# Optimization experiments

Hardware: AMD Instinct MI355X
Metric: run time of the kernel (lower is better)

## Reference

```python
import jax, jax.numpy as jnp
import numpy as np

BS, S, D, H, DFF, L = 8, 1024, 256, 8, 1024, 3
DK = D // H
NEG = -1e32


def setup_inputs() -> dict:
    key = jax.random.key(0)
    ks = jax.random.split(key, 10)
    r = lambda k, shp: jax.random.normal(k, shp, jnp.float32) * 0.02
    return {
        "q_embed_data": jax.random.normal(ks[0], (BS, S, D), jnp.float32),
        "qa_embed_data": jax.random.normal(ks[1], (BS, S, D), jnp.float32),
        "Wk": r(ks[2], (L, D, D)), "bk": jnp.zeros((L, D), jnp.float32),
        "Wv": r(ks[3], (L, D, D)), "bv": jnp.zeros((L, D), jnp.float32),
        "Wo": r(ks[4], (L, D, D)), "bo": jnp.zeros((L, D), jnp.float32),
        "gammas": r(ks[5], (L, H)),
        "ln1_g": jnp.ones((L, D), jnp.float32), "ln1_b": jnp.zeros((L, D), jnp.float32),
        "W1": r(ks[6], (L, D, DFF)), "b1": jnp.zeros((L, DFF), jnp.float32),
        "W2": r(ks[7], (L, DFF, D)), "b2": jnp.zeros((L, D), jnp.float32),
        "ln2_g": jnp.ones((L, D), jnp.float32), "ln2_b": jnp.zeros((L, D), jnp.float32),
    }


def _layernorm(x, g, b, eps=1e-5):
    mu = x.mean(-1, keepdims=True)
    var = ((x - mu) ** 2).mean(-1, keepdims=True)
    return (x - mu) * jax.lax.rsqrt(var + eps) * g + b


def _attn(xq, xk, xv, Wk, bk, Wv, bv, Wo, bo, gamma, mask, zero_pad):
    # kq_same=1: q and k both use k_linear
    bs = xq.shape[0]
    q = (xq @ Wk + bk).reshape(bs, S, H, DK).transpose(0, 2, 1, 3)  # bhsd
    k = (xk @ Wk + bk).reshape(bs, S, H, DK).transpose(0, 2, 1, 3)
    v = (xv @ Wv + bv).reshape(bs, S, H, DK).transpose(0, 2, 1, 3)
    scores = jnp.einsum('bhid,bhjd->bhij', q, k) / np.float32(np.sqrt(DK))
    mf = mask.astype(scores.dtype)
    # no-grad decay branch (detached in torch)
    p = jax.nn.softmax(jnp.where(mask, scores, NEG), axis=-1) * mf
    distcum = jnp.cumsum(p, axis=-1)
    disttot = p.sum(axis=-1, keepdims=True)
    idx = jnp.arange(S)
    pos = jnp.abs(idx[None, :] - idx[:, None]).astype(jnp.float32)[None, None]
    dist = jnp.sqrt(jnp.clip((disttot - distcum) * pos, 0.0, None))
    dist = jax.lax.stop_gradient(dist)
    g = -jax.nn.softplus(gamma)[None, :, None, None]  # (1,H,1,1)
    total_effect = jnp.clip(jnp.exp(dist * g), 1e-5, 1e5)
    scores = scores * total_effect
    attn = jax.nn.softmax(jnp.where(mask, scores, NEG), axis=-1)
    if zero_pad:
        attn = attn.at[:, :, 0, :].set(0.0)
    out = jnp.einsum('bhij,bhjd->bhid', attn, v)
    out = out.transpose(0, 2, 1, 3).reshape(bs, S, D)
    return out @ Wo + bo


def _block(i, xq, xk, xv, mask, zero_pad, apply_pos, P):
    Wk, bk, Wv, bv, Wo, bo, gam, l1g, l1b, W1, b1, W2, b2, l2g, l2b = [p[i] for p in P]
    q2 = _attn(xq, xk, xv, Wk, bk, Wv, bv, Wo, bo, gam, mask, zero_pad)
    x = _layernorm(xq + q2, l1g, l1b)
    if apply_pos:
        ff = jax.nn.relu(x @ W1 + b1) @ W2 + b2
        x = _layernorm(x + ff, l2g, l2b)
    return x


def _forward(q_embed_data, qa_embed_data, Wk, bk, Wv, bv, Wo, bo, gammas,
             ln1_g, ln1_b, W1, b1, W2, b2, ln2_g, ln2_b):
    P = (Wk, bk, Wv, bv, Wo, bo, gammas, ln1_g, ln1_b, W1, b1, W2, b2, ln2_g, ln2_b)
    tri_incl = jnp.tril(jnp.ones((S, S), bool))[None, None]       # mask=1: peek current+past
    tri_excl = jnp.tril(jnp.ones((S, S), bool), -1)[None, None]   # mask=0: strictly past
    x, y = q_embed_data, qa_embed_data
    # blocks_1 (n_blocks=1): mask=1, apply_pos=True, self-attn on y
    y = _block(0, y, y, y, tri_incl, False, True, P)
    # blocks_2 (2*n_blocks=2): alternate (mask=1, no FFN) / (mask=0, zero_pad, FFN, values=y)
    x = _block(1, x, x, x, tri_incl, False, False, P)
    x = _block(2, x, x, y, tri_excl, True, True, P)
    return x


def reference(q_embed_data, qa_embed_data, Wk, bk, Wv, bv, Wo, bo, gammas,
              ln1_g, ln1_b, W1, b1, W2, b2, ln2_g, ln2_b):
    return _forward(q_embed_data, qa_embed_data, Wk, bk, Wv, bv, Wo, bo, gammas,
                    ln1_g, ln1_b, W1, b1, W2, b2, ln2_g, ln2_b)
```

## Files before the change

### kernel.cpp

```cpp
#include <hip/hip_runtime.h>

typedef unsigned short u16;
typedef float f32x4 __attribute__((ext_vector_type(4)));
typedef __bf16 bf16x8 __attribute__((ext_vector_type(8)));
typedef u16 u16x8 __attribute__((ext_vector_type(8)));
typedef u16 u16x4 __attribute__((ext_vector_type(4)));
typedef __fp16 h16x2 __attribute__((ext_vector_type(2)));

__device__ __forceinline__ u16 f2bf(float f) {
  union { float f; unsigned u; } v; v.f = f;
  unsigned r = (v.u + 0x7FFFu + ((v.u >> 16) & 1u)) >> 16;
  return (u16)r;
}
__device__ __forceinline__ unsigned cvtpk_bf16(float lo, float hi) {
  unsigned r;
  asm("v_cvt_pk_bf16_f32 %0, %1, %2" : "=v"(r) : "v"(lo), "v"(hi));
  return r;
}
__device__ __forceinline__ unsigned pk_f16(float a, float b) {
  union { h16x2 h; unsigned u; } v;
  v.h = __builtin_amdgcn_cvt_pkrtz(a, b);
  return v.u;
}
__device__ __forceinline__ float2 unpk_f16(unsigned u) {
  union { unsigned u; h16x2 h; } v; v.u = u;
  return make_float2((float)v.h.x, (float)v.h.y);
}
__device__ __forceinline__ float wred_sum(float v) {
#pragma unroll
  for (int o = 32; o >= 1; o >>= 1) v += __shfl_xor(v, o);
  return v;
}

template <int RELU, int WF32, int WBF, int WVT>
__global__ __launch_bounds__(256) void gemm_kernel(
    const u16* __restrict__ A, const u16* __restrict__ Bt,
    const float* __restrict__ bias, float* __restrict__ C,
    u16* __restrict__ Cbf, int M, int N, int K) {
  __shared__ u16 As[64 * 64];
  __shared__ u16 Bs[64 * 64];
  const int tid = threadIdx.x;
  const int lane = tid & 63;
  const int w = tid >> 6;
  const int m0 = blockIdx.x * 64;
  const int n0 = blockIdx.y * 64;
  const int wr = (w >> 1) * 32;
  const int wc = (w & 1) * 32;
  const int l15 = lane & 15, hi = lane >> 4;

  f32x4 acc[2][2] = {};

  for (int k0 = 0; k0 < K; k0 += 64) {
#pragma unroll
    for (int rep = 0; rep < 2; ++rep) {
      int idx = tid + rep * 256;
      int row = idx >> 3, c8 = idx & 7;
      int cs = ((c8 ^ (row & 7)) << 3);
      __builtin_amdgcn_global_load_lds(
          (const __attribute__((address_space(1))) void*)(A + (size_t)(m0 + row) * K + k0 + cs),
          (__attribute__((address_space(3))) void*)(&As[idx * 8]), 16, 0, 0);
      __builtin_amdgcn_global_load_lds(
          (const __attribute__((address_space(1))) void*)(Bt + (size_t)(n0 + row) * K + k0 + cs),
          (__attribute__((address_space(3))) void*)(&Bs[idx * 8]), 16, 0, 0);
    }
    __syncthreads();
#pragma unroll
    for (int kk = 0; kk < 2; ++kk) {
      int kb = (kk * 32 + (hi << 3)) << 1;
      bf16x8 af[2], bfr[2];
#pragma unroll
      for (int mf = 0; mf < 2; ++mf) {
        int m = wr + mf * 16 + l15;
        af[mf] = *(const bf16x8*)((const char*)As + m * 128 + (kb ^ ((m & 7) << 4)));
      }
#pragma unroll
      for (int nf = 0; nf < 2; ++nf) {
        int n = wc + nf * 16 + l15;
        bfr[nf] = *(const bf16x8*)((const char*)Bs + n * 128 + (kb ^ ((n & 7) << 4)));
      }
#pragma unroll
      for (int mf = 0; mf < 2; ++mf)
#pragma unroll
        for (int nf = 0; nf < 2; ++nf)
          acc[mf][nf] = __builtin_amdgcn_mfma_f32_16x16x32_bf16(af[mf], bfr[nf], acc[mf][nf], 0, 0, 0);
    }
    __syncthreads();
  }

#pragma unroll
  for (int mf = 0; mf < 2; ++mf)
#pragma unroll
    for (int nf = 0; nf < 2; ++nf) {
      int col = n0 + wc + nf * 16 + l15;
      float bia = bias[col];
      u16x4 tv;
#pragma unroll
      for (int r = 0; r < 4; ++r) {
        int row = m0 + wr + mf * 16 + (hi << 2) + r;
        float val = acc[mf][nf][r] + bia;
        if (RELU) val = fmaxf(val, 0.f);
        if (WF32) C[(size_t)row * N + col] = val;
        if (WBF) Cbf[(size_t)row * N + col] = f2bf(val);
        if (WVT) tv[r] = f2bf(val);
      }
      if (WVT) {
        int row0 = m0 + wr + mf * 16 + (hi << 2);
        size_t addr = (((size_t)(row0 >> 10) * 8 + (col >> 5)) * 32 + (col & 31)) * 1024 + (row0 & 1023);
        *(u16x4*)(Cbf + addr) = tv;
      }
    }
}

__global__ __launch_bounds__(256) void gemm_kv_kernel(
    const u16* __restrict__ A, const u16* __restrict__ Bt,
    const float* __restrict__ biasK, const float* __restrict__ biasV,
    u16* __restrict__ qkbf, u16* __restrict__ vT, int M, int N, int K) {
  __shared__ u16 As[64 * 64];
  __shared__ u16 Bs[64 * 64];
  const int tid = threadIdx.x;
  const int lane = tid & 63;
  const int w = tid >> 6;
  const int m0 = blockIdx.x * 64;
  const int n0 = blockIdx.y * 64;
  const int wr = (w >> 1) * 32;
  const int wc = (w & 1) * 32;
  const int l15 = lane & 15, hi = lane >> 4;

  f32x4 acc[2][2] = {};

  for (int k0 = 0; k0 < K; k0 += 64) {
#pragma unroll
    for (int rep = 0; rep < 2; ++rep) {
      int idx = tid + rep * 256;
      int row = idx >> 3, c8 = idx & 7;
      int cs = ((c8 ^ (row & 7)) << 3);
      __builtin_amdgcn_global_load_lds(
          (const __attribute__((address_space(1))) void*)(A + (size_t)(m0 + row) * K + k0 + cs),
          (__attribute__((address_space(3))) void*)(&As[idx * 8]), 16, 0, 0);
      __builtin_amdgcn_global_load_lds(
          (const __attribute__((address_space(1))) void*)(Bt + (size_t)(n0 + row) * K + k0 + cs),
          (__attribute__((address_space(3))) void*)(&Bs[idx * 8]), 16, 0, 0);
    }
    __syncthreads();
#pragma unroll
    for (int kk = 0; kk < 2; ++kk) {
      int kb = (kk * 32 + (hi << 3)) << 1;
      bf16x8 af[2], bfr[2];
#pragma unroll
      for (int mf = 0; mf < 2; ++mf) {
        int m = wr + mf * 16 + l15;
        af[mf] = *(const bf16x8*)((const char*)As + m * 128 + (kb ^ ((m & 7) << 4)));
      }
#pragma unroll
      for (int nf = 0; nf < 2; ++nf) {
        int n = wc + nf * 16 + l15;
        bfr[nf] = *(const bf16x8*)((const char*)Bs + n * 128 + (kb ^ ((n & 7) << 4)));
      }
#pragma unroll
      for (int mf = 0; mf < 2; ++mf)
#pragma unroll
        for (int nf = 0; nf < 2; ++nf)
          acc[mf][nf] = __builtin_amdgcn_mfma_f32_16x16x32_bf16(af[mf], bfr[nf], acc[mf][nf], 0, 0, 0);
    }
    __syncthreads();
  }

  const bool isV = (n0 >= 256);
#pragma unroll
  for (int mf = 0; mf < 2; ++mf)
#pragma unroll
    for (int nf = 0; nf < 2; ++nf) {
      int col = n0 + wc + nf * 16 + l15;
      float bia = isV ? biasV[col - 256] : biasK[col];
      u16x4 tv;
#pragma unroll
      for (int r = 0; r < 4; ++r) {
        int row = m0 + wr + mf * 16 + (hi << 2) + r;
        float val = acc[mf][nf][r] + bia;
        if (!isV) qkbf[(size_t)row * 256 + col] = f2bf(val);
        tv[r] = f2bf(val);
      }
      if (isV) {
        int row0 = m0 + wr + mf * 16 + (hi << 2);
        int vc = col - 256;
        size_t addr = (((size_t)(row0 >> 10) * 8 + (vc >> 5)) * 32 + (vc & 31)) * 1024 + (row0 & 1023);
        *(u16x4*)(vT + addr) = tv;
      }
    }
}

__global__ __launch_bounds__(256) void attn_mfma_kernel(
    const u16* __restrict__ qkbf, const u16* __restrict__ vT,
    u16* __restrict__ ao, const float* __restrict__ gam, int excl) {
  __shared__ float zbuf[4][16];
  __shared__ float z2buf[4][16];
  __shared__ float accbuf[8][4][64];

  const int lane = threadIdx.x & 63, w = threadIdx.x >> 6;
  const int qt = 63 - blockIdx.y;
  const int bh = blockIdx.x;
  const int b = bh >> 3, h = bh & 7;
  const int q0 = qt * 16;
  const int l15 = lane & 15, hi = lane >> 4;
  const int i = q0 + l15;
  const float LOG2E = 1.4426950408889634f;
  const float g2 = -log1pf(__expf(gam[h])) * LOG2E;
  const float cscale = 0.17677669529663687f * LOG2E;
  const float CLIP2 = -16.609640474436812f;

  const u16* kbase = qkbf + ((size_t)b * 1024) * 256 + h * 32;
  const bf16x8 qfrag = *(const bf16x8*)(kbase + (size_t)i * 256 + hi * 8);

  const int mylim = i - excl;
  const int jmax = q0 + 15 - excl;
  const int ntiles = (jmax >> 4) + 1;
  const int C = (ntiles + 3) >> 2;
  const int c0 = w * C;
  const int tEnd = (c0 + C < ntiles) ? (c0 + C) : ntiles;
  const int count = (tEnd > c0) ? (tEnd - c0) : 0;

  unsigned lpk[32];
  float zacc = 0.f;
#pragma unroll
  for (int tl = 0; tl < 16; ++tl) {
    if (tl < count) {
      const int t = c0 + tl;
      bf16x8 kf = *(const bf16x8*)(kbase + (size_t)(t * 16 + l15) * 256 + hi * 8);
      f32x4 sA = {};
      sA = __builtin_amdgcn_mfma_f32_16x16x32_bf16(kf, qfrag, sA, 0, 0, 0);
      float l0 = sA[0] * cscale, l1 = sA[1] * cscale;
      float l2 = sA[2] * cscale, l3 = sA[3] * cscale;
      if (t == ntiles - 1) {
        const int kb = t * 16 + hi * 4;
        l0 = (kb + 0 <= mylim) ? l0 : -1000.f;
        l1 = (kb + 1 <= mylim) ? l1 : -1000.f;
        l2 = (kb + 2 <= mylim) ? l2 : -1000.f;
        l3 = (kb + 3 <= mylim) ? l3 : -1000.f;
      }
      zacc += (exp2f(l0) + exp2f(l1)) + (exp2f(l2) + exp2f(l3));
      lpk[2 * tl] = pk_f16(l0, l1);
      lpk[2 * tl + 1] = pk_f16(l2, l3);
    } else {
      lpk[2 * tl] = 0xE3D0E3D0u;
      lpk[2 * tl + 1] = 0xE3D0E3D0u;
    }
  }
  zacc += __shfl_xor(zacc, 16);
  zacc += __shfl_xor(zacc, 32);
  if (lane < 16) zbuf[w][lane] = zacc;
  __syncthreads();

  const float zc0 = zbuf[0][l15], zc1 = zbuf[1][l15];
  const float zc2 = zbuf[2][l15], zc3 = zbuf[3][l15];
  const float Z = zc0 + zc1 + zc2 + zc3;
  const float invZ = Z > 0.f ? 1.f / Z : 0.f;
  float prefix = 0.f;
  if (w > 0) prefix += zc0;
  if (w > 1) prefix += zc1;
  if (w > 2) prefix += zc2;

  const u16* vbase = vT + (size_t)bh * 32 * 1024;
  float carry = prefix, z2 = 0.f;
  f32x4 accO0 = {}, accO1 = {};
  const int Cp = (count + 1) & ~1;

  auto tile_sm = [&](int tlocal, unsigned pa, unsigned pb,
                     unsigned& u0, unsigned& u1) {
    float2 v01 = unpk_f16(pa), v23 = unpk_f16(pb);
    const float l0 = v01.x, l1 = v01.y, l2 = v23.x, l3 = v23.y;
    const float e0 = exp2f(l0), e1 = exp2f(l1);
    const float e2 = exp2f(l2), e3 = exp2f(l3);
    const float cA = e0 + e1, cB = cA + e2, cC = cB + e3;
    float vsc = cC;
    float tmp = __shfl_up(vsc, 16); if (hi >= 1) vsc += tmp;
    tmp = __shfl_up(vsc, 32); if (hi >= 2) vsc += tmp;
    const float exg = vsc - cC;
    const float tot = __shfl(vsc, l15 + 48);
    const float cb = carry + exg;
    carry += tot;
    const int kb = (c0 + tlocal) * 16 + hi * 4;
    const float posb = (float)(i - kb);
    const float r0 = (Z - (cb + e0)) * invZ;
    const float r1 = (Z - (cb + cA)) * invZ;
    const float r2 = (Z - (cb + cB)) * invZ;
    const float r3 = (Z - (cb + cC)) * invZ;
    const float d20 = fmaxf(r0 * posb, 0.f);
    const float d21 = fmaxf(r1 * (posb - 1.f), 0.f);
    const float d22 = fmaxf(r2 * (posb - 2.f), 0.f);
    const float d23 = fmaxf(r3 * (posb - 3.f), 0.f);
    const float a0 = fmaxf(__builtin_amdgcn_sqrtf(d20) * g2, CLIP2);
    const float a1 = fmaxf(__builtin_amdgcn_sqrtf(d21) * g2, CLIP2);
    const float a2 = fmaxf(__builtin_amdgcn_sqrtf(d22) * g2, CLIP2);
    const float a3 = fmaxf(__builtin_amdgcn_sqrtf(d23) * g2, CLIP2);
    const float p0 = exp2f(l0 * exp2f(a0));
    const float p1 = exp2f(l1 * exp2f(a1));
    const float p2 = exp2f(l2 * exp2f(a2));
    const float p3 = exp2f(l3 * exp2f(a3));
    z2 += (p0 + p1) + (p2 + p3);
    u0 = cvtpk_bf16(p0, p1);
    u1 = cvtpk_bf16(p2, p3);
  };

#pragma unroll
  for (int pp = 0; pp < 8; ++pp) {
    if (2 * pp < Cp) {
      unsigned pk00, pk01, u0, u1;
      tile_sm(2 * pp, lpk[4 * pp], lpk[4 * pp + 1], pk00, pk01);
      tile_sm(2 * pp + 1, lpk[4 * pp + 2], lpk[4 * pp + 3], u0, u1);
      const int srcA = l15 + (((2 * hi) & 3) << 4);
      const int srcB = l15 + (((2 * hi + 1) & 3) << 4);
      unsigned a00 = (unsigned)__shfl((int)pk00, srcA);
      unsigned a01 = (unsigned)__shfl((int)u0,   srcA);
      unsigned a10 = (unsigned)__shfl((int)pk01, srcA);
      unsigned a11 = (unsigned)__shfl((int)u1,   srcA);
      unsigned b00 = (unsigned)__shfl((int)pk00, srcB);
      unsigned b01 = (unsigned)__shfl((int)u0,   srcB);
      unsigned b10 = (unsigned)__shfl((int)pk01, srcB);
      unsigned b11 = (unsigned)__shfl((int)u1,   srcB);
      const bool up = hi >= 2;
      union { unsigned u[4]; bf16x8 v; } pf;
      pf.u[0] = up ? a01 : a00;
      pf.u[1] = up ? a11 : a10;
      pf.u[2] = up ? b01 : b00;
      pf.u[3] = up ? b11 : b10;
      const int jb = (c0 + 2 * pp) * 16;
      bf16x8 vf0 = *(const bf16x8*)(vbase + (size_t)l15 * 1024 + jb + hi * 8);
      bf16x8 vf1 = *(const bf16x8*)(vbase + (size_t)(16 + l15) * 1024 + jb + hi * 8);
      accO0 = __builtin_amdgcn_mfma_f32_16x16x32_bf16(vf0, pf.v, accO0, 0, 0, 0);
      accO1 = __builtin_amdgcn_mfma_f32_16x16x32_bf16(vf1, pf.v, accO1, 0, 0, 0);
    }
  }

  z2 += __shfl_xor(z2, 16);
  z2 += __shfl_xor(z2, 32);
  if (lane < 16) z2buf[w][lane] = z2;
#pragma unroll
  for (int j = 0; j < 4; ++j) {
    accbuf[j][w][lane] = accO0[j];
    accbuf[4 + j][w][lane] = accO1[j];
  }
  __syncthreads();

  if (w == 0) {
    const float z2t = z2buf[0][l15] + z2buf[1][l15] + z2buf[2][l15] + z2buf[3][l15];
    const float inv2 = z2t > 0.f ? 1.f / z2t : 0.f;
    u16* aop = ao + ((size_t)(b * 1024 + i)) * 256 + h * 32;
    float s0[4], s1[4];
#pragma unroll
    for (int j = 0; j < 4; ++j) {
      s0[j] = (accbuf[j][0][lane] + accbuf[j][1][lane] + accbuf[j][2][lane] + accbuf[j][3][lane]) * inv2;
      s1[j] = (accbuf[4 + j][0][lane] + accbuf[4 + j][1][lane] + accbuf[4 + j][2][lane] + accbuf[4 + j][3][lane]) * inv2;
    }
    uint2 o0, o1;
    o0.x = cvtpk_bf16(s0[0], s0[1]); o0.y = cvtpk_bf16(s0[2], s0[3]);
    o1.x = cvtpk_bf16(s1[0], s1[1]); o1.y = cvtpk_bf16(s1[2], s1[3]);
    *(uint2*)(aop + hi * 4) = o0;
    *(uint2*)(aop + 16 + hi * 4) = o1;
  }
}

__global__ __launch_bounds__(256) void add_ln_kernel(
    const float* __restrict__ res, const float* __restrict__ add,
    const float* __restrict__ g, const float* __restrict__ b,
    float* __restrict__ outf, u16* __restrict__ outb) {
  const int lane = threadIdx.x & 63, wid = threadIdx.x >> 6;
  const size_t row = (size_t)blockIdx.x * 4 + wid;
  const size_t base = row * 256 + lane * 4;
  float4 rv = *(const float4*)(res + base);
  float4 av = *(const float4*)(add + base);
  float x0 = rv.x + av.x, x1 = rv.y + av.y, x2 = rv.z + av.z, x3 = rv.w + av.w;
  float sm = wred_sum(x0 + x1 + x2 + x3);
  float mu = sm * (1.f / 256.f);
  float d0 = x0 - mu, d1 = x1 - mu, d2 = x2 - mu, d3 = x3 - mu;
  float vs = wred_sum(d0 * d0 + d1 * d1 + d2 * d2 + d3 * d3);
  float rs = rsqrtf(vs * (1.f / 256.f) + 1e-5f);
  float4 gv = *(const float4*)(g + lane * 4);
  float4 bv = *(const float4*)(b + lane * 4);
  float o0 = d0 * rs * gv.x + bv.x;
  float o1 = d1 * rs * gv.y + bv.y;
  float o2 = d2 * rs * gv.z + bv.z;
  float o3 = d3 * rs * gv.w + bv.w;
  float4 ov = {o0, o1, o2, o3};
  *(float4*)(outf + base) = ov;
  u16x4 wv; wv[0] = f2bf(o0); wv[1] = f2bf(o1); wv[2] = f2bf(o2); wv[3] = f2bf(o3);
  *(u16x4*)(outb + base) = wv;
}

__global__ __launch_bounds__(256) void cast_bf_kernel(
    const float* __restrict__ in, u16* __restrict__ out) {
  size_t i = ((size_t)blockIdx.x * 256 + threadIdx.x) * 8;
  float4 a = *(const float4*)(in + i);
  float4 c = *(const float4*)(in + i + 4);
  u16x8 o;
  o[0] = f2bf(a.x); o[1] = f2bf(a.y); o[2] = f2bf(a.z); o[3] = f2bf(a.w);
  o[4] = f2bf(c.x); o[5] = f2bf(c.y); o[6] = f2bf(c.z); o[7] = f2bf(c.w);
  *(u16x8*)(out + i) = o;
}

__global__ __launch_bounds__(256) void transpose_cast_kernel(
    const float* __restrict__ W, u16* __restrict__ Wt, int K, int N,
    int dstStride) {
  __shared__ float t[32][33];
  const size_t lo = (size_t)blockIdx.z * K * N;
  const size_t lod = (size_t)blockIdx.z * dstStride;
  int n0 = blockIdx.x * 32, k0 = blockIdx.y * 32;
  int tx = threadIdx.x, ty = threadIdx.y;
#pragma unroll
  for (int r = 0; r < 32; r += 8)
    t[ty + r][tx] = W[lo + (size_t)(k0 + ty + r) * N + n0 + tx];
  __syncthreads();
#pragma unroll
  for (int r = 0; r < 32; r += 8)
    Wt[lod + (size_t)(n0 + ty + r) * K + k0 + tx] = f2bf(t[tx][ty + r]);
}

extern "C" void kernel_launch(void* const* d_in, const int* in_sizes, int n_in,
                              void* d_out, int out_size, void* d_ws,
                              size_t ws_size, hipStream_t stream) {
  const float* q_embed = (const float*)d_in[0];
  const float* qa_embed = (const float*)d_in[1];
  const float* Wk = (const float*)d_in[2];
  const float* bk = (const float*)d_in[3];
  const float* Wv = (const float*)d_in[4];
  const float* bv = (const float*)d_in[5];
  const float* Wo = (const float*)d_in[6];
  const float* bo = (const float*)d_in[7];
  const float* gammas = (const float*)d_in[8];
  const float* ln1_g = (const float*)d_in[9];
  const float* ln1_b = (const float*)d_in[10];
  const float* W1 = (const float*)d_in[11];
  const float* b1 = (const float*)d_in[12];
  const float* W2 = (const float*)d_in[13];
  const float* b2 = (const float*)d_in[14];
  const float* ln2_g = (const float*)d_in[15];
  const float* ln2_b = (const float*)d_in[16];

  const size_t ACT_F32 = (size_t)8192 * 256 * 4;
  const size_t ACT_BF = (size_t)8192 * 256 * 2;
  char* p = (char*)d_ws;
  auto carve = [&](size_t bytes) {
    void* r = (void*)p;
    p += (bytes + 255) & ~(size_t)255;
    return r;
  };
  float* yb = (float*)carve(ACT_F32);
  float* xb = (float*)carve(ACT_F32);
  float* pof = (float*)carve(ACT_F32);
  u16* xbf = (u16*)carve(ACT_BF);
  u16* ybf = (u16*)carve(ACT_BF);
  u16* qkbf = (u16*)carve(ACT_BF);
  u16* vTb = (u16*)carve(ACT_BF);
  u16* aobf = (u16*)carve(ACT_BF);
  u16* hbf = (u16*)carve((size_t)8192 * 1024 * 2);
  u16* Wkvt = (u16*)carve((size_t)3 * 131072 * 2);
  u16* Wot = (u16*)carve((size_t)3 * 65536 * 2);
  u16* W1t = (u16*)carve((size_t)3 * 262144 * 2);
  u16* W2t = (u16*)carve((size_t)3 * 262144 * 2);

  dim3 tb(32, 8);
  transpose_cast_kernel<<<dim3(8, 8, 3), tb, 0, stream>>>(Wk, Wkvt, 256, 256, 131072);
  transpose_cast_kernel<<<dim3(8, 8, 3), tb, 0, stream>>>(Wv, Wkvt + 65536, 256, 256, 131072);
  transpose_cast_kernel<<<dim3(8, 8, 3), tb, 0, stream>>>(Wo, Wot, 256, 256, 65536);
  transpose_cast_kernel<<<dim3(32, 8, 3), tb, 0, stream>>>(W1, W1t, 256, 1024, 262144);
  transpose_cast_kernel<<<dim3(8, 32, 3), tb, 0, stream>>>(W2, W2t, 1024, 256, 262144);
  cast_bf_kernel<<<1024, 256, 0, stream>>>(q_embed, xbf);
  cast_bf_kernel<<<1024, 256, 0, stream>>>(qa_embed, ybf);

  const dim3 gP(128, 4), gF(128, 16), gKV(128, 8);
  const dim3 gA(64, 64);

  gemm_kv_kernel<<<gKV, 256, 0, stream>>>(ybf, Wkvt, bk, bv, qkbf, vTb, 8192, 512, 256);
  attn_mfma_kernel<<<gA, 256, 0, stream>>>(qkbf, vTb, aobf, gammas, 0);
  gemm_kernel<0, 1, 0, 0><<<gP, 256, 0, stream>>>(aobf, Wot, bo, pof, nullptr, 8192, 256, 256);
  add_ln_kernel<<<2048, 256, 0, stream>>>(qa_embed, pof, ln1_g, ln1_b, yb, ybf);
  gemm_kernel<1, 0, 1, 0><<<gF, 256, 0, stream>>>(ybf, W1t, b1, nullptr, hbf, 8192, 1024, 256);
  gemm_kernel<0, 1, 0, 0><<<gP, 256, 0, stream>>>(hbf, W2t, b2, pof, nullptr, 8192, 256, 1024);
  add_ln_kernel<<<2048, 256, 0, stream>>>(yb, pof, ln2_g, ln2_b, yb, ybf);

  gemm_kv_kernel<<<gKV, 256, 0, stream>>>(xbf, Wkvt + 131072, bk + 256, bv + 256, qkbf, vTb, 8192, 512, 256);
  attn_mfma_kernel<<<gA, 256, 0, stream>>>(qkbf, vTb, aobf, gammas + 8, 0);
  gemm_kernel<0, 1, 0, 0><<<gP, 256, 0, stream>>>(aobf, Wot + 65536, bo + 256, pof, nullptr, 8192, 256, 256);
  add_ln_kernel<<<2048, 256, 0, stream>>>(q_embed, pof, ln1_g + 256, ln1_b + 256, xb, xbf);

  gemm_kv_kernel<<<gKV, 256, 0, stream>>>(xbf, Wkvt + 262144, bk + 512, bv + 512, qkbf, vTb, 8192, 512, 256);
  gemm_kernel<0, 0, 0, 1><<<gP, 256, 0, stream>>>(ybf, Wkvt + 262144 + 65536, bv + 512, nullptr, vTb, 8192, 256, 256);
  attn_mfma_kernel<<<gA, 256, 0, stream>>>(qkbf, vTb, aobf, gammas + 16, 1);
  gemm_kernel<0, 1, 0, 0><<<gP, 256, 0, stream>>>(aobf, Wot + 131072, bo + 512, pof, nullptr, 8192, 256, 256);
  add_ln_kernel<<<2048, 256, 0, stream>>>(xb, pof, ln1_g + 512, ln1_b + 512, xb, xbf);
  gemm_kernel<1, 0, 1, 0><<<gF, 256, 0, stream>>>(xbf, W1t + 524288, b1 + 2048, nullptr, hbf, 8192, 1024, 256);
  gemm_kernel<0, 1, 0, 0><<<gP, 256, 0, stream>>>(hbf, W2t + 524288, b2 + 512, pof, nullptr, 8192, 256, 1024);
  add_ln_kernel<<<2048, 256, 0, stream>>>(xb, pof, ln2_g + 512, ln2_b + 512, (float*)d_out, xbf);
}
```

Before: 298.3 us.

## Pair short and long query tiles per attention block and recompute scores

Each attention block now handles two query tiles, qp and 63-qp, so every block has about the same causal work. Two waves split the combined tile range between them. The fp16 register cache of logits from the first pass is removed; QK^T scores are recomputed with MFMA in the second pass instead. This balances load across blocks and frees registers, at the cost of a second K load and MFMA per tile plus dynamic, non-unrolled loops.

```diff
diff --git a/kernel.cpp b/kernel.cpp
--- a/kernel.cpp
+++ b/kernel.cpp
@@ -5,7 +5,6 @@
 typedef __bf16 bf16x8 __attribute__((ext_vector_type(8)));
 typedef u16 u16x8 __attribute__((ext_vector_type(8)));
 typedef u16 u16x4 __attribute__((ext_vector_type(4)));
-typedef __fp16 h16x2 __attribute__((ext_vector_type(2)));
 
 __device__ __forceinline__ u16 f2bf(float f) {
   union { float f; unsigned u; } v; v.f = f;
@@ -16,15 +15,6 @@
   unsigned r;
   asm("v_cvt_pk_bf16_f32 %0, %1, %2" : "=v"(r) : "v"(lo), "v"(hi));
   return r;
-}
-__device__ __forceinline__ unsigned pk_f16(float a, float b) {
-  union { h16x2 h; unsigned u; } v;
-  v.h = __builtin_amdgcn_cvt_pkrtz(a, b);
-  return v.u;
-}
-__device__ __forceinline__ float2 unpk_f16(unsigned u) {
-  union { unsigned u; h16x2 h; } v; v.u = u;
-  return make_float2((float)v.h.x, (float)v.h.y);
 }
 __device__ __forceinline__ float wred_sum(float v) {
 #pragma unroll
@@ -189,88 +179,83 @@
     }
 }
 
-__global__ __launch_bounds__(256) void attn_mfma_kernel(
+__global__ __launch_bounds__(128) void attn_mfma_kernel(
     const u16* __restrict__ qkbf, const u16* __restrict__ vT,
     u16* __restrict__ ao, const float* __restrict__ gam, int excl) {
-  __shared__ float zbuf[4][16];
-  __shared__ float z2buf[4][16];
-  __shared__ float accbuf[8][4][64];
+  __shared__ float zbufA[2][16], zbufB[2][16];
+  __shared__ float z2bufA[2][16], z2bufB[2][16];
+  __shared__ float accbufA[8][2][64], accbufB[8][2][64];
 
   const int lane = threadIdx.x & 63, w = threadIdx.x >> 6;
-  const int qt = 63 - blockIdx.y;
-  const int bh = blockIdx.x;
+  const int qp = blockIdx.y, bh = blockIdx.x;
   const int b = bh >> 3, h = bh & 7;
-  const int q0 = qt * 16;
+  const int qtA = qp, qtB = 63 - qp;
+  const int q0A = qtA * 16, q0B = qtB * 16;
   const int l15 = lane & 15, hi = lane >> 4;
-  const int i = q0 + l15;
+  const int iA = q0A + l15, iB = q0B + l15;
   const float LOG2E = 1.4426950408889634f;
   const float g2 = -log1pf(__expf(gam[h])) * LOG2E;
   const float cscale = 0.17677669529663687f * LOG2E;
   const float CLIP2 = -16.609640474436812f;
 
-  const u16* kbase = qkbf + ((size_t)b * 1024) * 256 + h * 32;
-  const bf16x8 qfrag = *(const bf16x8*)(kbase + (size_t)i * 256 + hi * 8);
-
-  const int mylim = i - excl;
-  const int jmax = q0 + 15 - excl;
-  const int ntiles = (jmax >> 4) + 1;
-  const int C = (ntiles + 3) >> 2;
-  const int c0 = w * C;
-  const int tEnd = (c0 + C < ntiles) ? (c0 + C) : ntiles;
-  const int count = (tEnd > c0) ? (tEnd - c0) : 0;
-
-  unsigned lpk[32];
-  float zacc = 0.f;
-#pragma unroll
-  for (int tl = 0; tl < 16; ++tl) {
-    if (tl < count) {
-      const int t = c0 + tl;
-      bf16x8 kf = *(const bf16x8*)(kbase + (size_t)(t * 16 + l15) * 256 + hi * 8);
-      f32x4 sA = {};
-      sA = __builtin_amdgcn_mfma_f32_16x16x32_bf16(kf, qfrag, sA, 0, 0, 0);
-      float l0 = sA[0] * cscale, l1 = sA[1] * cscale;
-      float l2 = sA[2] * cscale, l3 = sA[3] * cscale;
-      if (t == ntiles - 1) {
-        const int kb = t * 16 + hi * 4;
-        l0 = (kb + 0 <= mylim) ? l0 : -1000.f;
-        l1 = (kb + 1 <= mylim) ? l1 : -1000.f;
-        l2 = (kb + 2 <= mylim) ? l2 : -1000.f;
-        l3 = (kb + 3 <= mylim) ? l3 : -1000.f;
-      }
-      zacc += (exp2f(l0) + exp2f(l1)) + (exp2f(l2) + exp2f(l3));
-      lpk[2 * tl] = pk_f16(l0, l1);
-      lpk[2 * tl + 1] = pk_f16(l2, l3);
-    } else {
-      lpk[2 * tl] = 0xE3D0E3D0u;
-      lpk[2 * tl + 1] = 0xE3D0E3D0u;
-    }
-  }
-  zacc += __shfl_xor(zacc, 16);
-  zacc += __shfl_xor(zacc, 32);
-  if (lane < 16) zbuf[w][lane] = zacc;
+  const u16* kbase = qkbf + (size_t)b * 1024 * 256 + h * 32;
+  const u16* vbase = vT + (size_t)bh * 32 * 1024;
+  const bf16x8 qfragA = *(const bf16x8*)(kbase + (size_t)iA * 256 + hi * 8);
+  const bf16x8 qfragB = *(const bf16x8*)(kbase + (size_t)iB * 256 + hi * 8);
+
+  const int mylimA = iA - excl, mylimB = iB - excl;
+  const int ntA = qtA + 1, ntB = qtB + 1;
+  const int ntT = ntA + ntB;
+  const int C = (ntT + 1) >> 1;
+  const int g0 = w * C;
+  const int g1e = g0 + C < ntT ? g0 + C : ntT;
+  const int aS = g0 < ntA ? g0 : ntA;
+  const int aE = g1e < ntA ? g1e : ntA;
+  const int bS = (g0 > ntA ? g0 : ntA) - ntA;
+  const int bE = (g1e > ntA ? g1e : ntA) - ntA;
+
+  auto calc_l = [&](const bf16x8& qf, int t, int lastT, int mylim, float* l) {
+    bf16x8 kf = *(const bf16x8*)(kbase + (size_t)(t * 16 + l15) * 256 + hi * 8);
+    f32x4 sA = {};
+    sA = __builtin_amdgcn_mfma_f32_16x16x32_bf16(kf, qf, sA, 0, 0, 0);
+    l[0] = sA[0] * cscale; l[1] = sA[1] * cscale;
+    l[2] = sA[2] * cscale; l[3] = sA[3] * cscale;
+    if (t == lastT) {
+      const int kb = t * 16 + hi * 4;
+      l[0] = (kb + 0 <= mylim) ? l[0] : -1000.f;
+      l[1] = (kb + 1 <= mylim) ? l[1] : -1000.f;
+      l[2] = (kb + 2 <= mylim) ? l[2] : -1000.f;
+      l[3] = (kb + 3 <= mylim) ? l[3] : -1000.f;
+    }
+  };
+
+  float zA = 0.f, zB = 0.f;
+  for (int t = aS; t < aE; ++t) {
+    float l[4]; calc_l(qfragA, t, ntA - 1, mylimA, l);
+    zA += (exp2f(l[0]) + exp2f(l[1])) + (exp2f(l[2]) + exp2f(l[3]));
+  }
+  for (int t = bS; t < bE; ++t) {
+    float l[4]; calc_l(qfragB, t, ntB - 1, mylimB, l);
+    zB += (exp2f(l[0]) + exp2f(l[1])) + (exp2f(l[2]) + exp2f(l[3]));
+  }
+  zA += __shfl_xor(zA, 16); zA += __shfl_xor(zA, 32);
+  zB += __shfl_xor(zB, 16); zB += __shfl_xor(zB, 32);
+  if (lane < 16) { zbufA[w][lane] = zA; zbufB[w][lane] = zB; }
   __syncthreads();
 
-  const float zc0 = zbuf[0][l15], zc1 = zbuf[1][l15];
-  const float zc2 = zbuf[2][l15], zc3 = zbuf[3][l15];
-  const float Z = zc0 + zc1 + zc2 + zc3;
-  const float invZ = Z > 0.f ? 1.f / Z : 0.f;
-  float prefix = 0.f;
-  if (w > 0) prefix += zc0;
-  if (w > 1) prefix += zc1;
-  if (w > 2) prefix += zc2;
-
-  const u16* vbase = vT + (size_t)bh * 32 * 1024;
-  float carry = prefix, z2 = 0.f;
-  f32x4 accO0 = {}, accO1 = {};
-  const int Cp = (count + 1) & ~1;
-
-  auto tile_sm = [&](int tlocal, unsigned pa, unsigned pb,
-                     unsigned& u0, unsigned& u1) {
-    float2 v01 = unpk_f16(pa), v23 = unpk_f16(pb);
-    const float l0 = v01.x, l1 = v01.y, l2 = v23.x, l3 = v23.y;
-    const float e0 = exp2f(l0), e1 = exp2f(l1);
-    const float e2 = exp2f(l2), e3 = exp2f(l3);
-    const float cA = e0 + e1, cB = cA + e2, cC = cB + e3;
+  const float zA0 = zbufA[0][l15], zA1 = zbufA[1][l15];
+  const float zB0 = zbufB[0][l15], zB1 = zbufB[1][l15];
+  const float ZA = zA0 + zA1, ZB = zB0 + zB1;
+  const float invZA = ZA > 0.f ? 1.f / ZA : 0.f;
+  const float invZB = ZB > 0.f ? 1.f / ZB : 0.f;
+  const float prefA = (w > 0) ? zA0 : 0.f;
+  const float prefB = (w > 0) ? zB0 : 0.f;
+
+  auto sm4 = [&](const float* l, int kb, int irow, float Z, float invZ,
+                 float& carry, float& z2) -> uint2 {
+    const float e0 = exp2f(l[0]), e1 = exp2f(l[1]);
+    const float e2 = exp2f(l[2]), e3 = exp2f(l[3]);
+    const float cA = e0 + e1, cB2 = cA + e2, cC = cB2 + e3;
     float vsc = cC;
     float tmp = __shfl_up(vsc, 16); if (hi >= 1) vsc += tmp;
     tmp = __shfl_up(vsc, 32); if (hi >= 2) vsc += tmp;
@@ -278,11 +263,10 @@
     const float tot = __shfl(vsc, l15 + 48);
     const float cb = carry + exg;
     carry += tot;
-    const int kb = (c0 + tlocal) * 16 + hi * 4;
-    const float posb = (float)(i - kb);
+    const float posb = (float)(irow - kb);
     const float r0 = (Z - (cb + e0)) * invZ;
     const float r1 = (Z - (cb + cA)) * invZ;
-    const float r2 = (Z - (cb + cB)) * invZ;
+    const float r2 = (Z - (cb + cB2)) * invZ;
     const float r3 = (Z - (cb + cC)) * invZ;
     const float d20 = fmaxf(r0 * posb, 0.f);
     const float d21 = fmaxf(r1 * (posb - 1.f), 0.f);
@@ -292,64 +276,81 @@
     const float a1 = fmaxf(__builtin_amdgcn_sqrtf(d21) * g2, CLIP2);
     const float a2 = fmaxf(__builtin_amdgcn_sqrtf(d22) * g2, CLIP2);
     const float a3 = fmaxf(__builtin_amdgcn_sqrtf(d23) * g2, CLIP2);
-    const float p0 = exp2f(l0 * exp2f(a0));
-    const float p1 = exp2f(l1 * exp2f(a1));
-    const float p2 = exp2f(l2 * exp2f(a2));
-    const float p3 = exp2f(l3 * exp2f(a3));
+    const float p0 = exp2f(l[0] * exp2f(a0));
+    const float p1 = exp2f(l[1] * exp2f(a1));
+    const float p2 = exp2f(l[2] * exp2f(a2));
+    const float p3 = exp2f(l[3] * exp2f(a3));
     z2 += (p0 + p1) + (p2 + p3);
-    u0 = cvtpk_bf16(p0, p1);
-    u1 = cvtpk_bf16(p2, p3);
+    uint2 r; r.x = cvtpk_bf16(p0, p1); r.y = cvtpk_bf16(p2, p3);
+    return r;
   };
 
-#pragma unroll
-  for (int pp = 0; pp < 8; ++pp) {
-    if (2 * pp < Cp) {
-      unsigned pk00, pk01, u0, u1;
-      tile_sm(2 * pp, lpk[4 * pp], lpk[4 * pp + 1], pk00, pk01);
-      tile_sm(2 * pp + 1, lpk[4 * pp + 2], lpk[4 * pp + 3], u0, u1);
+  auto run_ctx = [&](int s, int e, int lastT, int mylim, const bf16x8& qf,
+                     int irow, float Z, float invZ, float& carry, float& z2,
+                     f32x4& acc0, f32x4& acc1) {
+    for (int t0 = s; t0 < e; t0 += 2) {
+      const int t1 = t0 + 1;
+      float la[4], lb[4];
+      calc_l(qf, t0, lastT, mylim, la);
+      const bool v1 = (t1 < e);
+      if (v1) calc_l(qf, t1, lastT, mylim, lb);
+      uint2 uA = sm4(la, t0 * 16 + hi * 4, irow, Z, invZ, carry, z2);
+      uint2 uB = make_uint2(0u, 0u);
+      if (v1) uB = sm4(lb, t1 * 16 + hi * 4, irow, Z, invZ, carry, z2);
       const int srcA = l15 + (((2 * hi) & 3) << 4);
       const int srcB = l15 + (((2 * hi + 1) & 3) << 4);
-      unsigned a00 = (unsigned)__shfl((int)pk00, srcA);
-      unsigned a01 = (unsigned)__shfl((int)u0,   srcA);
-      unsigned a10 = (unsigned)__shfl((int)pk01, srcA);
-      unsigned a11 = (unsigned)__shfl((int)u1,   srcA);
-      unsigned b00 = (unsigned)__shfl((int)pk00, srcB);
-      unsigned b01 = (unsigned)__shfl((int)u0,   srcB);
-      unsigned b10 = (unsigned)__shfl((int)pk01, srcB);
-      unsigned b11 = (unsigned)__shfl((int)u1,   srcB);
+      unsigned a00 = (unsigned)__shfl((int)uA.x, srcA);
+      unsigned a01 = (unsigned)__shfl((int)uB.x, srcA);
+      unsigned a10 = (unsigned)__shfl((int)uA.y, srcA);
+      unsigned a11 = (unsigned)__shfl((int)uB.y, srcA);
+      unsigned b00 = (unsigned)__shfl((int)uA.x, srcB);
+      unsigned b01 = (unsigned)__shfl((int)uB.x, srcB);
+      unsigned b10 = (unsigned)__shfl((int)uA.y, srcB);
+      unsigned b11 = (unsigned)__shfl((int)uB.y, srcB);
       const bool up = hi >= 2;
       union { unsigned u[4]; bf16x8 v; } pf;
       pf.u[0] = up ? a01 : a00;
       pf.u[1] = up ? a11 : a10;
       pf.u[2] = up ? b01 : b00;
       pf.u[3] = up ? b11 : b10;
-      const int jb = (c0 + 2 * pp) * 16;
+      const int jb = t0 * 16;
       bf16x8 vf0 = *(const bf16x8*)(vbase + (size_t)l15 * 1024 + jb + hi * 8);
       bf16x8 vf1 = *(const bf16x8*)(vbase + (size_t)(16 + l15) * 1024 + jb + hi * 8);
-      accO0 = __builtin_amdgcn_mfma_f32_16x16x32_bf16(vf0, pf.v, accO0, 0, 0, 0);
-      accO1 = __builtin_amdgcn_mfma_f32_16x16x32_bf16(vf1, pf.v, accO1, 0, 0, 0);
-    }
-  }
-
-  z2 += __shfl_xor(z2, 16);
-  z2 += __shfl_xor(z2, 32);
-  if (lane < 16) z2buf[w][lane] = z2;
+      acc0 = __builtin_amdgcn_mfma_f32_16x16x32_bf16(vf0, pf.v, acc0, 0, 0, 0);
+      acc1 = __builtin_amdgcn_mfma_f32_16x16x32_bf16(vf1, pf.v, acc1, 0, 0, 0);
+    }
+  };
+
+  float carryA = prefA, z2A = 0.f, carryB = prefB, z2B = 0.f;
+  f32x4 aA0 = {}, aA1 = {}, aB0 = {}, aB1 = {};
+  run_ctx(aS, aE, ntA - 1, mylimA, qfragA, iA, ZA, invZA, carryA, z2A, aA0, aA1);
+  run_ctx(bS, bE, ntB - 1, mylimB, qfragB, iB, ZB, invZB, carryB, z2B, aB0, aB1);
+
+  z2A += __shfl_xor(z2A, 16); z2A += __shfl_xor(z2A, 32);
+  z2B += __shfl_xor(z2B, 16); z2B += __shfl_xor(z2B, 32);
+  if (lane < 16) { z2bufA[w][lane] = z2A; z2bufB[w][lane] = z2B; }
 #pragma unroll
   for (int j = 0; j < 4; ++j) {
-    accbuf[j][w][lane] = accO0[j];
-    accbuf[4 + j][w][lane] = accO1[j];
+    accbufA[j][w][lane] = aA0[j];
+    accbufA[4 + j][w][lane] = aA1[j];
+    accbufB[j][w][lane] = aB0[j];
+    accbufB[4 + j][w][lane] = aB1[j];
   }
   __syncthreads();
 
-  if (w == 0) {
-    const float z2t = z2buf[0][l15] + z2buf[1][l15] + z2buf[2][l15] + z2buf[3][l15];
+  {
+    const bool isA = (w == 0);
+    float (*z2p)[16] = isA ? z2bufA : z2bufB;
+    float (*accp)[2][64] = isA ? accbufA : accbufB;
+    const int irow = isA ? iA : iB;
+    const float z2t = z2p[0][l15] + z2p[1][l15];
     const float inv2 = z2t > 0.f ? 1.f / z2t : 0.f;
-    u16* aop = ao + ((size_t)(b * 1024 + i)) * 256 + h * 32;
+    u16* aop = ao + ((size_t)(b * 1024 + irow)) * 256 + h * 32;
     float s0[4], s1[4];
 #pragma unroll
     for (int j = 0; j < 4; ++j) {
-      s0[j] = (accbuf[j][0][lane] + accbuf[j][1][lane] + accbuf[j][2][lane] + accbuf[j][3][lane]) * inv2;
-      s1[j] = (accbuf[4 + j][0][lane] + accbuf[4 + j][1][lane] + accbuf[4 + j][2][lane] + accbuf[4 + j][3][lane]) * inv2;
+      s0[j] = (accp[j][0][lane] + accp[j][1][lane]) * inv2;
+      s1[j] = (accp[4 + j][0][lane] + accp[4 + j][1][lane]) * inv2;
     }
     uint2 o0, o1;
     o0.x = cvtpk_bf16(s0[0], s0[1]); o0.y = cvtpk_bf16(s0[2], s0[3]);
@@ -467,10 +468,10 @@
   cast_bf_kernel<<<1024, 256, 0, stream>>>(qa_embed, ybf);
 
   const dim3 gP(128, 4), gF(128, 16), gKV(128, 8);
-  const dim3 gA(64, 64);
+  const dim3 gA(64, 32);
 
   gemm_kv_kernel<<<gKV, 256, 0, stream>>>(ybf, Wkvt, bk, bv, qkbf, vTb, 8192, 512, 256);
-  attn_mfma_kernel<<<gA, 256, 0, stream>>>(qkbf, vTb, aobf, gammas, 0);
+  attn_mfma_kernel<<<gA, 128, 0, stream>>>(qkbf, vTb, aobf, gammas, 0);
   gemm_kernel<0, 1, 0, 0><<<gP, 256, 0, stream>>>(aobf, Wot, bo, pof, nullptr, 8192, 256, 256);
   add_ln_kernel<<<2048, 256, 0, stream>>>(qa_embed, pof, ln1_g, ln1_b, yb, ybf);
   gemm_kernel<1, 0, 1, 0><<<gF, 256, 0, stream>>>(ybf, W1t, b1, nullptr, hbf, 8192, 1024, 256);
@@ -478,13 +479,13 @@
   add_ln_kernel<<<2048, 256, 0, stream>>>(yb, pof, ln2_g, ln2_b, yb, ybf);
 
   gemm_kv_kernel<<<gKV, 256, 0, stream>>>(xbf, Wkvt + 131072, bk + 256, bv + 256, qkbf, vTb, 8192, 512, 256);
-  attn_mfma_kernel<<<gA, 256, 0, stream>>>(qkbf, vTb, aobf, gammas + 8, 0);
+  attn_mfma_kernel<<<gA, 128, 0, stream>>>(qkbf, vTb, aobf, gammas + 8, 0);
   gemm_kernel<0, 1, 0, 0><<<gP, 256, 0, stream>>>(aobf, Wot + 65536, bo + 256, pof, nullptr, 8192, 256, 256);
   add_ln_kernel<<<2048, 256, 0, stream>>>(q_embed, pof, ln1_g + 256, ln1_b + 256, xb, xbf);
 
   gemm_kv_kernel<<<gKV, 256, 0, stream>>>(xbf, Wkvt + 262144, bk + 512, bv + 512, qkbf, vTb, 8192, 512, 256);
   gemm_kernel<0, 0, 0, 1><<<gP, 256, 0, stream>>>(ybf, Wkvt + 262144 + 65536, bv + 512, nullptr, vTb, 8192, 256, 256);
-  attn_mfma_kernel<<<gA, 256, 0, stream>>>(qkbf, vTb, aobf, gammas + 16, 1);
+  attn_mfma_kernel<<<gA, 128, 0, stream>>>(qkbf, vTb, aobf, gammas + 16, 1);
   gemm_kernel<0, 1, 0, 0><<<gP, 256, 0, stream>>>(aobf, Wot + 131072, bo + 512, pof, nullptr, 8192, 256, 256);
   add_ln_kernel<<<2048, 256, 0, stream>>>(xb, pof, ln1_g + 512, ln1_b + 512, xb, xbf);
   gemm_kernel<1, 0, 1, 0><<<gF, 256, 0, stream>>>(xbf, W1t + 524288, b1 + 2048, nullptr, hbf, 8192, 1024, 256);
```

After: 336.2 us. 12.7% more time.
